# Kernel optimization log

Measured on AMD Instinct MI355X. Metric: run time of the kernel, lower is better.

Reference implementation:

```python
import jax, jax.numpy as jnp
import numpy as np

B, S, D = 2, 2048, 2048
H, DK, DV, LD = 16, 128, 128, 64


def setup_inputs() -> dict:
    key = jax.random.key(0)
    ks = jax.random.split(key, 12)
    s = lambda fan_in: 1.0 / np.sqrt(fan_in)
    return {
        "queries": jax.random.normal(ks[0], (B, S, D), jnp.float32),
        "keys": jax.random.normal(ks[1], (B, S, D), jnp.float32),
        "values": jax.random.normal(ks[2], (B, S, D), jnp.float32),
        # linear_q: Linear(D, DK*H)
        "Wq": jax.random.uniform(ks[3], (D, DK * H), jnp.float32, -s(D), s(D)),
        "bq": jax.random.uniform(ks[4], (DK * H,), jnp.float32, -s(D), s(D)),
        # latent_k_proj / latent_v_proj: Linear(D, LD*H)
        "Wlk": jax.random.uniform(ks[5], (D, LD * H), jnp.float32, -s(D), s(D)),
        "blk": jax.random.uniform(ks[6], (LD * H,), jnp.float32, -s(D), s(D)),
        "Wlv": jax.random.uniform(ks[7], (D, LD * H), jnp.float32, -s(D), s(D)),
        "blv": jax.random.uniform(ks[8], (LD * H,), jnp.float32, -s(D), s(D)),
        # k/v reconstruction: Linear(LD, DK/DV, bias=False), stored [LD, DK]
        "Wkr": jax.random.uniform(ks[9], (LD, DK), jnp.float32, -s(LD), s(LD)),
        "Wvr": jax.random.uniform(ks[10], (LD, DV), jnp.float32, -s(LD), s(LD)),
        # linear_out: Linear(DV*H, D)
        "Wout": jax.random.uniform(ks[11], (DV * H, D), jnp.float32, -s(DV * H), s(DV * H)),
        "bout": jnp.zeros((D,), jnp.float32),
    }


def reference(queries, keys, values, Wq, bq, Wlk, blk, Wlv, blv, Wkr, Wvr, Wout, bout):
    b, sq, _ = queries.shape
    sk = keys.shape[1]
    # Q projection -> [b, H, sq, DK]
    q = (queries @ Wq + bq).reshape(b, sq, H, DK).transpose(0, 2, 1, 3)
    # Low-rank latent K/V -> [b, H, sk, LD]
    lk = (keys @ Wlk + blk).reshape(b, sk, H, LD).transpose(0, 2, 1, 3)
    lv = (values @ Wlv + blv).reshape(b, sk, H, LD).transpose(0, 2, 1, 3)
    # Reconstruct full K/V from latents -> [b, H, sk, DK/DV]
    k = lk @ Wkr
    v = lv @ Wvr
    scores = jnp.einsum('bhqd,bhkd->bhqk', q, k) / np.sqrt(DK).astype(np.float32)
    causal = jnp.triu(jnp.ones((sq, sk), dtype=bool), k=1)
    scores = jnp.where(causal, -jnp.inf, scores)
    attn = jax.nn.softmax(scores, axis=-1)
    out = jnp.einsum('bhqk,bhkd->bhqd', attn, v)  # [b, H, sq, DV]
    out = out.transpose(0, 2, 1, 3).reshape(b, sq, H * DV)
    return out @ Wout + bout
```

## Files before the change

kernel.cpp:

```cpp
#include <hip/hip_runtime.h>

#define S_LEN 2048
#define NH 16

typedef unsigned short u16;
typedef __attribute__((ext_vector_type(8))) short bf16x8;
typedef __attribute__((ext_vector_type(4))) short s16x4;
typedef __attribute__((ext_vector_type(4))) unsigned short u16x4;
typedef __attribute__((ext_vector_type(4))) unsigned int u32x4;
typedef __attribute__((ext_vector_type(4))) float f32x4;

__device__ __forceinline__ u16 f2bf(float f) {
  union { float f; unsigned int i; } x; x.f = f;
  unsigned int r = x.i + 0x7FFFu + ((x.i >> 16) & 1u);
  return (u16)(r >> 16);
}
__device__ __forceinline__ unsigned pk2(float lo, float hi) {
  unsigned r;
  asm("v_cvt_pk_bf16_f32 %0, %1, %2" : "=v"(r) : "v"(lo), "v"(hi));
  return r;
}
__device__ __forceinline__ void glds16(const void* g, void* l) {
  __builtin_amdgcn_global_load_lds((const __attribute__((address_space(1))) void*)g,
                                   (__attribute__((address_space(3))) void*)l, 16, 0, 0);
}

__global__ __launch_bounds__(256) void cast3_f32_bf16(const float* __restrict__ i0,
                                                      const float* __restrict__ i1,
                                                      const float* __restrict__ i2,
                                                      u16* __restrict__ o0,
                                                      u16* __restrict__ o1,
                                                      u16* __restrict__ o2) {
  int z = blockIdx.y;
  const float* in = z == 0 ? i0 : (z == 1 ? i1 : i2);
  u16* out = z == 0 ? o0 : (z == 1 ? o1 : o2);
  size_t i = ((size_t)blockIdx.x * 256 + threadIdx.x) * 8;
  f32x4 a = *(const f32x4*)&in[i];
  f32x4 b = *(const f32x4*)&in[i + 4];
  u32x4 o;
  o[0] = pk2(a[0], a[1]);
  o[1] = pk2(a[2], a[3]);
  o[2] = pk2(b[0], b[1]);
  o[3] = pk2(b[2], b[3]);
  *(u32x4*)&out[i] = o;
}

__global__ __launch_bounds__(256) void cast_f32_bf16(const float* __restrict__ in,
                                                     u16* __restrict__ out) {
  size_t i = ((size_t)blockIdx.x * 256 + threadIdx.x) * 8;
  f32x4 a = *(const f32x4*)&in[i];
  f32x4 b = *(const f32x4*)&in[i + 4];
  u32x4 o;
  o[0] = pk2(a[0], a[1]);
  o[1] = pk2(a[2], a[3]);
  o[2] = pk2(b[0], b[1]);
  o[3] = pk2(b[2], b[3]);
  *(u32x4*)&out[i] = o;
}

__global__ __launch_bounds__(256) void cast2_f32_bf16(const float* __restrict__ i0,
                                                      const float* __restrict__ i1,
                                                      u16* __restrict__ o0,
                                                      u16* __restrict__ o1) {
  const float* in = blockIdx.y ? i1 : i0;
  u16* out = blockIdx.y ? o1 : o0;
  size_t i = ((size_t)blockIdx.x * 256 + threadIdx.x) * 8;
  f32x4 a = *(const f32x4*)&in[i];
  f32x4 b = *(const f32x4*)&in[i + 4];
  u32x4 o;
  o[0] = pk2(a[0], a[1]);
  o[1] = pk2(a[2], a[3]);
  o[2] = pk2(b[0], b[1]);
  o[3] = pk2(b[2], b[3]);
  *(u32x4*)&out[i] = o;
}

__global__ __launch_bounds__(256) void transpose2_f32_bf16(const float* __restrict__ i0,
                                                           const float* __restrict__ i1,
                                                           u16* __restrict__ o0,
                                                           u16* __restrict__ o1,
                                                           int K, int N) {
  const float* in = blockIdx.z ? i1 : i0;
  u16* out = blockIdx.z ? o1 : o0;
  __shared__ u16 tile[64][72];
  int k0 = blockIdx.y * 64, n0 = blockIdx.x * 64;
  int t = threadIdx.x;
#pragma unroll
  for (int i = 0; i < 4; ++i) {
    int idx = i * 256 + t;
    int r = idx >> 4;
    int c4 = (idx & 15) << 2;
    f32x4 v = *(const f32x4*)&in[(size_t)(k0 + r) * N + n0 + c4];
#pragma unroll
    for (int j = 0; j < 4; ++j) tile[r][c4 + j] = f2bf(v[j]);
  }
  __syncthreads();
#pragma unroll
  for (int i = 0; i < 4; ++i) {
    int idx = i * 256 + t;
    int r = idx >> 4;
    int c4 = (idx & 15) << 2;
    u16x4 v;
    v[0] = tile[c4 + 0][r];
    v[1] = tile[c4 + 1][r];
    v[2] = tile[c4 + 2][r];
    v[3] = tile[c4 + 3][r];
    *(u16x4*)&out[(size_t)(n0 + r) * K + k0 + c4] = v;
  }
}

__global__ __launch_bounds__(256) void transpose_f32_bf16(const float* __restrict__ in,
                                                          u16* __restrict__ out,
                                                          int K, int N) {
  __shared__ u16 tile[64][72];
  int k0 = blockIdx.y * 64, n0 = blockIdx.x * 64;
  int t = threadIdx.x;
#pragma unroll
  for (int i = 0; i < 4; ++i) {
    int idx = i * 256 + t;
    int r = idx >> 4;
    int c4 = (idx & 15) << 2;
    f32x4 v = *(const f32x4*)&in[(size_t)(k0 + r) * N + n0 + c4];
#pragma unroll
    for (int j = 0; j < 4; ++j) tile[r][c4 + j] = f2bf(v[j]);
  }
  __syncthreads();
#pragma unroll
  for (int i = 0; i < 4; ++i) {
    int idx = i * 256 + t;
    int r = idx >> 4;
    int c4 = (idx & 15) << 2;
    u16x4 v;
    v[0] = tile[c4 + 0][r];
    v[1] = tile[c4 + 1][r];
    v[2] = tile[c4 + 2][r];
    v[3] = tile[c4 + 3][r];
    *(u16x4*)&out[(size_t)(n0 + r) * K + k0 + c4] = v;
  }
}

__global__ __launch_bounds__(256) void absorb_q(const u16* __restrict__ Wkr,
                                                const u16* __restrict__ Wqb,
                                                u16* __restrict__ Wq2T) {
  int kb = blockIdx.x, h = blockIdx.y;
  int t = threadIdx.x, w = t >> 6, lane = t & 63, lq = lane & 15, hi = lane >> 4;
  int k0 = kb * 128 + w * 32;
  f32x4 acc[4][2];
#pragma unroll
  for (int i = 0; i < 4; ++i)
#pragma unroll
    for (int j = 0; j < 2; ++j) acc[i][j] = (f32x4){0.f, 0.f, 0.f, 0.f};
#pragma unroll
  for (int kk = 0; kk < 4; ++kk) {
    bf16x8 a[4], bb[2];
#pragma unroll
    for (int fld = 0; fld < 4; ++fld)
      a[fld] = *(const bf16x8*)&Wkr[(fld * 16 + lq) * 128 + kk * 32 + hi * 8];
#pragma unroll
    for (int fk = 0; fk < 2; ++fk)
      bb[fk] = *(const bf16x8*)&Wqb[(size_t)(k0 + fk * 16 + lq) * 2048 + h * 128 + kk * 32 + hi * 8];
#pragma unroll
    for (int fld = 0; fld < 4; ++fld)
#pragma unroll
      for (int fk = 0; fk < 2; ++fk)
        acc[fld][fk] = __builtin_amdgcn_mfma_f32_16x16x32_bf16(a[fld], bb[fk], acc[fld][fk], 0, 0, 0);
  }
#pragma unroll
  for (int fld = 0; fld < 4; ++fld)
#pragma unroll
    for (int fk = 0; fk < 2; ++fk)
#pragma unroll
      for (int r = 0; r < 4; ++r)
        Wq2T[(size_t)(h * 64 + fld * 16 + hi * 4 + r) * 2048 + k0 + fk * 16 + lq] =
            f2bf(acc[fld][fk][r]);
}

__global__ __launch_bounds__(256) void absorb_o(const u16* __restrict__ WoutT,
                                                const u16* __restrict__ Wvr,
                                                u16* __restrict__ W2T) {
  int nb = blockIdx.x, h = blockIdx.y;
  int t = threadIdx.x, w = t >> 6, lane = t & 63, lq = lane & 15, hi = lane >> 4;
  int n0 = nb * 128 + w * 32;
  f32x4 acc[2][4];
#pragma unroll
  for (int i = 0; i < 2; ++i)
#pragma unroll
    for (int j = 0; j < 4; ++j) acc[i][j] = (f32x4){0.f, 0.f, 0.f, 0.f};
#pragma unroll
  for (int kk = 0; kk < 4; ++kk) {
    bf16x8 a[2], bb[4];
#pragma unroll
    for (int fn = 0; fn < 2; ++fn)
      a[fn] = *(const bf16x8*)&WoutT[(size_t)(n0 + fn * 16 + lq) * 2048 + h * 128 + kk * 32 + hi * 8];
#pragma unroll
    for (int fld = 0; fld < 4; ++fld)
      bb[fld] = *(const bf16x8*)&Wvr[(fld * 16 + lq) * 128 + kk * 32 + hi * 8];
#pragma unroll
    for (int fn = 0; fn < 2; ++fn)
#pragma unroll
      for (int fld = 0; fld < 4; ++fld)
        acc[fn][fld] = __builtin_amdgcn_mfma_f32_16x16x32_bf16(a[fn], bb[fld], acc[fn][fld], 0, 0, 0);
  }
#pragma unroll
  for (int fn = 0; fn < 2; ++fn)
#pragma unroll
    for (int fld = 0; fld < 4; ++fld)
#pragma unroll
      for (int r = 0; r < 4; ++r)
        W2T[(size_t)(n0 + fn * 16 + hi * 4 + r) * 1024 + h * 64 + fld * 16 + lq] =
            f2bf(acc[fn][fld][r]);
}

__global__ __launch_bounds__(256) void absorb_bq(const float* __restrict__ bq,
                                                 const float* __restrict__ Wkr,
                                                 float* __restrict__ bq2) {
  int n = blockIdx.x * 256 + threadIdx.x;
  int h = n >> 6, ld = n & 63;
  float s = 0.f;
#pragma unroll 8
  for (int dk = 0; dk < 128; ++dk) s += bq[h * 128 + dk] * Wkr[ld * 128 + dk];
  bq2[n] = s;
}

template <bool OF32>
__global__ __launch_bounds__(512, 2) void gemm8p(const u16* __restrict__ A0,
                                                 const u16* __restrict__ A1,
                                                 const u16* __restrict__ A2,
                                                 const u16* __restrict__ W0,
                                                 const u16* __restrict__ W1,
                                                 const u16* __restrict__ W2,
                                                 const float* __restrict__ b0,
                                                 const float* __restrict__ b1,
                                                 const float* __restrict__ b2,
                                                 void* __restrict__ C0,
                                                 void* __restrict__ C1,
                                                 void* __restrict__ C2,
                                                 int N, int K) {
  __shared__ u16 lds[4][2][256 * 32];
  int z = blockIdx.z;
  const u16* A = z == 0 ? A0 : (z == 1 ? A1 : A2);
  const u16* Wt = z == 0 ? W0 : (z == 1 ? W1 : W2);
  const float* bias = z == 0 ? b0 : (z == 1 ? b1 : b2);
  void* Cv = z == 0 ? C0 : (z == 1 ? C1 : C2);

  int m0 = blockIdx.y * 256, n0 = blockIdx.x * 256;
  int t = threadIdx.x;
  int lane = t & 63, lq = lane & 15, hi = lane >> 4;
  int w = t >> 6, wm = w >> 2, wn = w & 3;
  int NT = K >> 5;

  auto stage = [&](int q, int kt) {
    u16* lA = &lds[q][0][0];
    u16* lB = &lds[q][1][0];
    int kb = kt * 32;
#pragma unroll
    for (int i = 0; i < 2; ++i) {
      int idx = i * 512 + t;
      int row = idx >> 2, c = idx & 3;
      glds16(&A[(size_t)(m0 + row) * K + kb + ((c ^ (row & 3)) << 3)], lA + idx * 8);
    }
#pragma unroll
    for (int i = 0; i < 2; ++i) {
      int idx = i * 512 + t;
      int row = idx >> 2, c = idx & 3;
      glds16(&Wt[(size_t)(n0 + row) * K + kb + ((c ^ (row & 3)) << 3)], lB + idx * 8);
    }
  };

  f32x4 acc[8][4];
#pragma unroll
  for (int im = 0; im < 8; ++im)
#pragma unroll
    for (int fn = 0; fn < 4; ++fn) acc[im][fn] = (f32x4){0.f, 0.f, 0.f, 0.f};

  stage(0, 0);
  stage(1, 1);
  asm volatile("s_waitcnt vmcnt(4)" ::: "memory");
  __builtin_amdgcn_s_barrier();

  for (int tt = 0; tt < NT; ++tt) {
    int q = tt & 3;
    if (tt + 2 < NT) stage((tt + 2) & 3, tt + 2);
    const u16* lA = &lds[q][0][0];
    const u16* lB = &lds[q][1][0];
    bf16x8 bf[4];
#pragma unroll
    for (int fn = 0; fn < 4; ++fn) {
      int row = wn * 64 + fn * 16 + lq;
      bf[fn] = *(const bf16x8*)&lB[row * 32 + ((hi ^ (row & 3)) << 3)];
    }
    __builtin_amdgcn_s_setprio(1);
#pragma unroll
    for (int im = 0; im < 8; ++im) {
      int row = wm * 128 + im * 16 + lq;
      bf16x8 af = *(const bf16x8*)&lA[row * 32 + ((hi ^ (row & 3)) << 3)];
#pragma unroll
      for (int fn = 0; fn < 4; ++fn)
        acc[im][fn] = __builtin_amdgcn_mfma_f32_16x16x32_bf16(af, bf[fn], acc[im][fn], 0, 0, 0);
    }
    __builtin_amdgcn_s_setprio(0);
    if (tt + 2 < NT)
      asm volatile("s_waitcnt vmcnt(4)" ::: "memory");
    else
      asm volatile("s_waitcnt vmcnt(0)" ::: "memory");
    __builtin_amdgcn_s_barrier();
  }

#pragma unroll
  for (int im = 0; im < 8; ++im)
#pragma unroll
    for (int fn = 0; fn < 4; ++fn) {
      int col = n0 + wn * 64 + fn * 16 + lq;
      float bv = bias[col];
      int rbase = m0 + wm * 128 + im * 16 + hi * 4;
#pragma unroll
      for (int r = 0; r < 4; ++r) {
        float v = acc[im][fn][r] + bv;
        if constexpr (OF32)
          ((float*)Cv)[(size_t)(rbase + r) * N + col] = v;
        else
          ((u16*)Cv)[(size_t)(rbase + r) * N + col] = f2bf(v);
      }
    }
}

__global__ __launch_bounds__(256) void transpose_lv(const u16* __restrict__ LV,
                                                    u16* __restrict__ out) {
  __shared__ u16 tile[64 * 72];
  int st = blockIdx.x, bh = blockIdx.y;
  int b = bh >> 4, h = bh & 15;
  int t = threadIdx.x;
  int s0 = st * 64;
#pragma unroll
  for (int i = 0; i < 2; ++i) {
    int idx = i * 256 + t;
    int sr = idx >> 3, c8 = idx & 7;
    bf16x8 v = *(const bf16x8*)&LV[(size_t)(b * S_LEN + s0 + sr) * 1024 + h * 64 + c8 * 8];
    int pos = (sr & 32) + ((sr & 12) << 1) + ((sr & 16) >> 2) + (sr & 3);
#pragma unroll
    for (int j = 0; j < 8; ++j) tile[(c8 * 8 + j) * 72 + pos] = (u16)v[j];
  }
  __syncthreads();
  u16* ob = out + (size_t)bh * 64 * S_LEN;
#pragma unroll
  for (int i = 0; i < 2; ++i) {
    int idx = i * 256 + t;
    int ld = idx >> 3, c8 = idx & 7;
    bf16x8 v = *(const bf16x8*)&tile[ld * 72 + c8 * 8];
    *(bf16x8*)&ob[(size_t)ld * S_LEN + s0 + c8 * 8] = v;
  }
}

__global__ __launch_bounds__(256) void mla_attn5(const u16* __restrict__ Qp,
                                                 const u16* __restrict__ LK,
                                                 const u16* __restrict__ LVt,
                                                 u16* __restrict__ O) {
  __shared__ u16 smem[16384];
  int Lb = blockIdx.x + blockIdx.y * 8;
  int half = Lb >> 9;
  int i0 = Lb & 511;
  int xcd = i0 & 7, ii = i0 >> 3;
  int bh = xcd * 4 + (ii & 3);
  int pr = ii >> 2;
  int qsup = half ? (31 - pr) : pr;
  int b = bh >> 4, h = bh & 15;
  int t = threadIdx.x, w = t >> 6, lane = t & 63, lq = lane & 15, hi = lane >> 4;
  int lq7 = lq & 7;

  const u16* Kb = LK + (size_t)b * S_LEN * 1024 + h * 64;
  const u16* Vb = LVt + (size_t)bh * 64 * S_LEN;
  const float scale = 0.08838834764831845f;

  auto stage = [&](int buf, int k0) {
    u16* lK = smem + buf * 4096;
    u16* lV = smem + 8192 + buf * 4096;
#pragma unroll
    for (int i = 0; i < 2; ++i) {
      int idx = i * 256 + t;
      int row = idx >> 3, c8 = idx & 7;
      glds16(Kb + (size_t)(k0 + row) * 1024 + ((c8 ^ (row & 7)) << 3), lK + idx * 8);
    }
#pragma unroll
    for (int i = 0; i < 2; ++i) {
      int idx = i * 256 + t;
      int row = idx >> 3, c8 = idx & 7;
      glds16(Vb + (size_t)row * S_LEN + k0 + ((c8 ^ (row & 7)) << 3), lV + idx * 8);
    }
  };

  int qb = qsup * 64;
  int nt = qsup + 1;
  int q0 = qb + w * 16;
  int kmax = q0 + 16;

  bf16x8 qf[2];
  {
    const u16* Qrow = Qp + (size_t)(b * S_LEN + q0 + lq) * 1024 + h * 64;
    qf[0] = *(const bf16x8*)&Qrow[hi * 8];
    qf[1] = *(const bf16x8*)&Qrow[32 + hi * 8];
  }

  f32x4 acc[4];
#pragma unroll
  for (int f = 0; f < 4; ++f) acc[f] = (f32x4){0.f, 0.f, 0.f, 0.f};
  float m = -1e30f, l = 0.f;

  stage(0, 0);
  __syncthreads();
  for (int tt = 0; tt < nt; ++tt) {
    int cur = tt & 1;
    if (tt + 1 < nt) stage(cur ^ 1, (tt + 1) * 64);
    int k0 = tt * 64;
    if (k0 < kmax) {
      const u16* lK = smem + cur * 4096;
      const u16* lV = smem + 8192 + cur * 4096;
      f32x4 sc[4];
#pragma unroll
      for (int kf = 0; kf < 4; ++kf) sc[kf] = (f32x4){0.f, 0.f, 0.f, 0.f};
      __builtin_amdgcn_s_setprio(1);
#pragma unroll
      for (int kf = 0; kf < 4; ++kf) {
        const u16* kr = lK + (kf * 16 + lq) * 64;
#pragma unroll
        for (int d0 = 0; d0 < 2; ++d0) {
          bf16x8 af = *(const bf16x8*)&kr[(((d0 << 2) + hi) ^ lq7) << 3];
          sc[kf] = __builtin_amdgcn_mfma_f32_16x16x32_bf16(af, qf[d0], sc[kf], 0, 0, 0);
        }
      }
      __builtin_amdgcn_s_setprio(0);
      int q = q0 + lq;
      float sv[16];
#pragma unroll
      for (int kf = 0; kf < 4; ++kf)
#pragma unroll
        for (int r = 0; r < 4; ++r) sv[kf * 4 + r] = sc[kf][r] * scale;
      if (k0 + 63 > q0) {
#pragma unroll
        for (int kf = 0; kf < 4; ++kf)
#pragma unroll
          for (int r = 0; r < 4; ++r)
            if (k0 + kf * 16 + hi * 4 + r > q) sv[kf * 4 + r] = -1e30f;
      }
      float tm = sv[0];
#pragma unroll
      for (int j = 1; j < 16; ++j) tm = fmaxf(tm, sv[j]);
      tm = fmaxf(tm, __shfl_xor(tm, 16));
      tm = fmaxf(tm, __shfl_xor(tm, 32));
      float p[16], ps = 0.f;
      if (__all(tm <= m + 8.f)) {
#pragma unroll
        for (int j = 0; j < 16; ++j) { p[j] = __expf(sv[j] - m); ps += p[j]; }
        ps += __shfl_xor(ps, 16);
        ps += __shfl_xor(ps, 32);
        l += ps;
      } else {
        float mnew = fmaxf(m, tm);
        float alpha = __expf(m - mnew);
#pragma unroll
        for (int j = 0; j < 16; ++j) { p[j] = __expf(sv[j] - mnew); ps += p[j]; }
        ps += __shfl_xor(ps, 16);
        ps += __shfl_xor(ps, 32);
        l = l * alpha + ps;
        m = mnew;
#pragma unroll
        for (int f = 0; f < 4; ++f) {
          acc[f][0] *= alpha; acc[f][1] *= alpha;
          acc[f][2] *= alpha; acc[f][3] *= alpha;
        }
      }
      bf16x8 pb[2];
#pragma unroll
      for (int ks = 0; ks < 2; ++ks) {
        union { u32x4 u; bf16x8 v; } pu;
#pragma unroll
        for (int wd = 0; wd < 4; ++wd) pu.u[wd] = pk2(p[ks * 8 + 2 * wd], p[ks * 8 + 2 * wd + 1]);
        pb[ks] = pu.v;
      }
      __builtin_amdgcn_s_setprio(1);
#pragma unroll
      for (int f = 0; f < 4; ++f) {
        const u16* vr = lV + (f * 16 + lq) * 64;
#pragma unroll
        for (int ks = 0; ks < 2; ++ks) {
          bf16x8 va = *(const bf16x8*)&vr[(((ks << 2) + hi) ^ lq7) << 3];
          acc[f] = __builtin_amdgcn_mfma_f32_16x16x32_bf16(va, pb[ks], acc[f], 0, 0, 0);
        }
      }
      __builtin_amdgcn_s_setprio(0);
    }
    __syncthreads();
  }
  {
    float inv = 1.f / l;
    int qloc = w * 16 + lq;
#pragma unroll
    for (int f = 0; f < 4; ++f)
#pragma unroll
      for (int r = 0; r < 4; ++r) {
        int col = f * 16 + hi * 4 + r;
        smem[qloc * 64 + (((col >> 3) ^ lq7) << 3) + (col & 7)] = f2bf(acc[f][r] * inv);
      }
  }
  __syncthreads();
#pragma unroll
  for (int i = 0; i < 2; ++i) {
    int cid = i * 256 + t;
    int q = cid >> 3, ch = cid & 7;
    bf16x8 v = *(const bf16x8*)&smem[q * 64 + ((ch ^ (q & 7)) << 3)];
    *(bf16x8*)&O[(size_t)(b * S_LEN + qb + q) * 1024 + h * 64 + (ch << 3)] = v;
  }
}

extern "C" void kernel_launch(void* const* d_in, const int* in_sizes, int n_in,
                              void* d_out, int out_size, void* d_ws, size_t ws_size,
                              hipStream_t stream) {
  const float* queries = (const float*)d_in[0];
  const float* keys    = (const float*)d_in[1];
  const float* values  = (const float*)d_in[2];
  const float* Wq      = (const float*)d_in[3];
  const float* bq      = (const float*)d_in[4];
  const float* Wlk     = (const float*)d_in[5];
  const float* blk     = (const float*)d_in[6];
  const float* Wlv     = (const float*)d_in[7];
  const float* blv     = (const float*)d_in[8];
  const float* Wkr     = (const float*)d_in[9];
  const float* Wvr     = (const float*)d_in[10];
  const float* Wout    = (const float*)d_in[11];
  const float* bout    = (const float*)d_in[12];

  u16* ws = (u16*)d_ws;
  u16* WqBf  = ws; ws += (size_t)2048 * 2048;
  u16* WkrBf = ws; ws += 64 * 128;
  u16* WvrBf = ws; ws += 64 * 128;
  u16* WoutT = ws; ws += (size_t)2048 * 2048;
  u16* WlkT  = ws; ws += (size_t)1024 * 2048;
  u16* WlvT  = ws; ws += (size_t)1024 * 2048;
  u16* Wq2T  = ws; ws += (size_t)1024 * 2048;
  u16* W2T   = ws; ws += (size_t)2048 * 1024;
  float* bq2 = (float*)ws; ws += 2048;
  u16* Qin   = ws; ws += (size_t)4096 * 2048;
  u16* Kin   = ws; ws += (size_t)4096 * 2048;
  u16* Vin   = ws; ws += (size_t)4096 * 2048;
  u16* Qp    = ws; ws += (size_t)4096 * 1024;
  u16* LKb   = ws; ws += (size_t)4096 * 1024;
  u16* LVb   = ws; ws += (size_t)4096 * 1024;
  u16* LVt = Kin;
  u16* Ob  = Qin;

  dim3 blk256(256);
  cast3_f32_bf16<<<dim3(4096, 3), blk256, 0, stream>>>(queries, keys, values, Qin, Kin, Vin);
  cast_f32_bf16<<<dim3(2048), blk256, 0, stream>>>(Wq, WqBf);
  cast2_f32_bf16<<<dim3(4, 2), blk256, 0, stream>>>(Wkr, Wvr, WkrBf, WvrBf);

  transpose2_f32_bf16<<<dim3(16, 32, 2), blk256, 0, stream>>>(Wlk, Wlv, WlkT, WlvT, 2048, 1024);
  transpose_f32_bf16<<<dim3(32, 32), blk256, 0, stream>>>(Wout, WoutT, 2048, 2048);

  absorb_q<<<dim3(16, 16), blk256, 0, stream>>>(WkrBf, WqBf, Wq2T);
  absorb_o<<<dim3(16, 16), blk256, 0, stream>>>(WoutT, WvrBf, W2T);
  absorb_bq<<<dim3(4), blk256, 0, stream>>>(bq, Wkr, bq2);

  gemm8p<false><<<dim3(4, 16, 3), dim3(512), 0, stream>>>(
      Qin, Kin, Vin, Wq2T, WlkT, WlvT, bq2, blk, blv, Qp, LKb, LVb, 1024, 2048);

  transpose_lv<<<dim3(32, 32), blk256, 0, stream>>>(LVb, LVt);

  mla_attn5<<<dim3(8, 128), blk256, 0, stream>>>(Qp, LKb, LVt, Ob);

  gemm8p<true><<<dim3(8, 16, 1), dim3(512), 0, stream>>>(
      Ob, Ob, Ob, W2T, W2T, W2T, bout, bout, bout, d_out, d_out, d_out, 2048, 1024);
}
```

Before: 211.2 us.

## Retile projection GEMMs to 128x256 with BK=64, triple buffering and XCD-aware block mapping

Replaces the 256x256 tile, BK=32, four-stage GEMM with a 128x256 tile, BK=64, three-stage version that uses an 8-way XOR swizzle. Blocks are launched on a flat 1D grid and remapped so that all N-tiles of the same A row panel land on the same XCD, which improves L2 reuse of A. The smaller M tile doubles the block count, for better CU occupancy on 256 CUs, and halves the accumulator registers. In exchange each block reuses the B tile over fewer rows, so more B traffic is loaded per unit of work.

```diff
diff --git a/kernel.cpp b/kernel.cpp
--- a/kernel.cpp
+++ b/kernel.cpp
@@ -223,96 +223,108 @@
 }
 
 template <bool OF32>
-__global__ __launch_bounds__(512, 2) void gemm8p(const u16* __restrict__ A0,
-                                                 const u16* __restrict__ A1,
-                                                 const u16* __restrict__ A2,
-                                                 const u16* __restrict__ W0,
-                                                 const u16* __restrict__ W1,
-                                                 const u16* __restrict__ W2,
-                                                 const float* __restrict__ b0,
-                                                 const float* __restrict__ b1,
-                                                 const float* __restrict__ b2,
-                                                 void* __restrict__ C0,
-                                                 void* __restrict__ C1,
-                                                 void* __restrict__ C2,
-                                                 int N, int K) {
-  __shared__ u16 lds[4][2][256 * 32];
-  int z = blockIdx.z;
+__global__ __launch_bounds__(512, 2) void gemm_dp(const u16* __restrict__ A0,
+                                                  const u16* __restrict__ A1,
+                                                  const u16* __restrict__ A2,
+                                                  const u16* __restrict__ W0,
+                                                  const u16* __restrict__ W1,
+                                                  const u16* __restrict__ W2,
+                                                  const float* __restrict__ b0,
+                                                  const float* __restrict__ b1,
+                                                  const float* __restrict__ b2,
+                                                  void* __restrict__ C0,
+                                                  void* __restrict__ C1,
+                                                  void* __restrict__ C2,
+                                                  int N, int K, int nxl) {
+  __shared__ u16 ldsA[3][128 * 64];
+  __shared__ u16 ldsB[3][256 * 64];
+
+  int Lb = blockIdx.x;
+  int xcd = Lb & 7, slot = Lb >> 3;
+  int panel = ((slot >> nxl) << 3) + xcd;
+  int x = slot & ((1 << nxl) - 1);
+  int z = panel >> 5, y = panel & 31;
+
   const u16* A = z == 0 ? A0 : (z == 1 ? A1 : A2);
   const u16* Wt = z == 0 ? W0 : (z == 1 ? W1 : W2);
   const float* bias = z == 0 ? b0 : (z == 1 ? b1 : b2);
   void* Cv = z == 0 ? C0 : (z == 1 ? C1 : C2);
 
-  int m0 = blockIdx.y * 256, n0 = blockIdx.x * 256;
+  int m0 = y * 128, n0 = x * 256;
   int t = threadIdx.x;
   int lane = t & 63, lq = lane & 15, hi = lane >> 4;
   int w = t >> 6, wm = w >> 2, wn = w & 3;
-  int NT = K >> 5;
+  int NT = K >> 6;
 
   auto stage = [&](int q, int kt) {
-    u16* lA = &lds[q][0][0];
-    u16* lB = &lds[q][1][0];
-    int kb = kt * 32;
+    u16* lA = &ldsA[q][0];
+    u16* lB = &ldsB[q][0];
+    int kb = kt * 64;
 #pragma unroll
     for (int i = 0; i < 2; ++i) {
       int idx = i * 512 + t;
-      int row = idx >> 2, c = idx & 3;
-      glds16(&A[(size_t)(m0 + row) * K + kb + ((c ^ (row & 3)) << 3)], lA + idx * 8);
-    }
-#pragma unroll
-    for (int i = 0; i < 2; ++i) {
+      int row = idx >> 3, c8 = idx & 7;
+      glds16(&A[(size_t)(m0 + row) * K + kb + ((c8 ^ (row & 7)) << 3)], lA + idx * 8);
+    }
+#pragma unroll
+    for (int i = 0; i < 4; ++i) {
       int idx = i * 512 + t;
-      int row = idx >> 2, c = idx & 3;
-      glds16(&Wt[(size_t)(n0 + row) * K + kb + ((c ^ (row & 3)) << 3)], lB + idx * 8);
+      int row = idx >> 3, c8 = idx & 7;
+      glds16(&Wt[(size_t)(n0 + row) * K + kb + ((c8 ^ (row & 7)) << 3)], lB + idx * 8);
     }
   };
 
-  f32x4 acc[8][4];
-#pragma unroll
-  for (int im = 0; im < 8; ++im)
+  f32x4 acc[4][4];
+#pragma unroll
+  for (int im = 0; im < 4; ++im)
 #pragma unroll
     for (int fn = 0; fn < 4; ++fn) acc[im][fn] = (f32x4){0.f, 0.f, 0.f, 0.f};
 
   stage(0, 0);
   stage(1, 1);
-  asm volatile("s_waitcnt vmcnt(4)" ::: "memory");
+  asm volatile("s_waitcnt vmcnt(6)" ::: "memory");
   __builtin_amdgcn_s_barrier();
 
   for (int tt = 0; tt < NT; ++tt) {
-    int q = tt & 3;
-    if (tt + 2 < NT) stage((tt + 2) & 3, tt + 2);
-    const u16* lA = &lds[q][0][0];
-    const u16* lB = &lds[q][1][0];
-    bf16x8 bf[4];
-#pragma unroll
-    for (int fn = 0; fn < 4; ++fn) {
-      int row = wn * 64 + fn * 16 + lq;
-      bf[fn] = *(const bf16x8*)&lB[row * 32 + ((hi ^ (row & 3)) << 3)];
-    }
+    int q = tt % 3;
+    if (tt + 2 < NT) stage((tt + 2) % 3, tt + 2);
+    const u16* lA = &ldsA[q][0];
+    const u16* lB = &ldsB[q][0];
+    bf16x8 bf[2][4];
+#pragma unroll
+    for (int kk = 0; kk < 2; ++kk)
+#pragma unroll
+      for (int fn = 0; fn < 4; ++fn) {
+        int row = wn * 64 + fn * 16 + lq;
+        bf[kk][fn] = *(const bf16x8*)&lB[row * 64 + (((kk * 4 + hi) ^ (row & 7)) << 3)];
+      }
     __builtin_amdgcn_s_setprio(1);
 #pragma unroll
-    for (int im = 0; im < 8; ++im) {
-      int row = wm * 128 + im * 16 + lq;
-      bf16x8 af = *(const bf16x8*)&lA[row * 32 + ((hi ^ (row & 3)) << 3)];
-#pragma unroll
-      for (int fn = 0; fn < 4; ++fn)
-        acc[im][fn] = __builtin_amdgcn_mfma_f32_16x16x32_bf16(af, bf[fn], acc[im][fn], 0, 0, 0);
+    for (int im = 0; im < 4; ++im) {
+      int row = wm * 64 + im * 16 + lq;
+#pragma unroll
+      for (int kk = 0; kk < 2; ++kk) {
+        bf16x8 af = *(const bf16x8*)&lA[row * 64 + (((kk * 4 + hi) ^ (row & 7)) << 3)];
+#pragma unroll
+        for (int fn = 0; fn < 4; ++fn)
+          acc[im][fn] = __builtin_amdgcn_mfma_f32_16x16x32_bf16(af, bf[kk][fn], acc[im][fn], 0, 0, 0);
+      }
     }
     __builtin_amdgcn_s_setprio(0);
     if (tt + 2 < NT)
-      asm volatile("s_waitcnt vmcnt(4)" ::: "memory");
+      asm volatile("s_waitcnt vmcnt(6)" ::: "memory");
     else
       asm volatile("s_waitcnt vmcnt(0)" ::: "memory");
     __builtin_amdgcn_s_barrier();
   }
 
 #pragma unroll
-  for (int im = 0; im < 8; ++im)
+  for (int im = 0; im < 4; ++im)
 #pragma unroll
     for (int fn = 0; fn < 4; ++fn) {
       int col = n0 + wn * 64 + fn * 16 + lq;
       float bv = bias[col];
-      int rbase = m0 + wm * 128 + im * 16 + hi * 4;
+      int rbase = m0 + wm * 64 + im * 16 + hi * 4;
 #pragma unroll
       for (int r = 0; r < 4; ++r) {
         float v = acc[im][fn][r] + bv;
@@ -559,13 +571,13 @@
   absorb_o<<<dim3(16, 16), blk256, 0, stream>>>(WoutT, WvrBf, W2T);
   absorb_bq<<<dim3(4), blk256, 0, stream>>>(bq, Wkr, bq2);
 
-  gemm8p<false><<<dim3(4, 16, 3), dim3(512), 0, stream>>>(
-      Qin, Kin, Vin, Wq2T, WlkT, WlvT, bq2, blk, blv, Qp, LKb, LVb, 1024, 2048);
+  gemm_dp<false><<<dim3(384), dim3(512), 0, stream>>>(
+      Qin, Kin, Vin, Wq2T, WlkT, WlvT, bq2, blk, blv, Qp, LKb, LVb, 1024, 2048, 2);
 
   transpose_lv<<<dim3(32, 32), blk256, 0, stream>>>(LVb, LVt);
 
   mla_attn5<<<dim3(8, 128), blk256, 0, stream>>>(Qp, LKb, LVt, Ob);
 
-  gemm8p<true><<<dim3(8, 16, 1), dim3(512), 0, stream>>>(
-      Ob, Ob, Ob, W2T, W2T, W2T, bout, bout, bout, d_out, d_out, d_out, 2048, 1024);
-}
+  gemm_dp<true><<<dim3(256), dim3(512), 0, stream>>>(
+      Ob, Ob, Ob, W2T, W2T, W2T, bout, bout, bout, d_out, d_out, d_out, 2048, 1024, 3);
+}
```

After: 227.7 us. 7.8% more time.
